# Performance work log

Hardware: AMD Instinct MI355X
Metric: run time of the kernel (lower is better)

The kernel has to match this reference:

```python
import jax, jax.numpy as jnp
import numpy as np

EMB = 1024
HEADS = 16
HEAD_DIM = EMB // HEADS  # 64


def setup_inputs() -> dict:
    key = jax.random.key(0)
    ks = jax.random.split(key, 11)
    B, S = 2, 2048
    scale = 1.0 / np.sqrt(EMB)
    inp = {
        "xv": jax.random.normal(ks[0], (B, S, EMB), jnp.float32),
        "xk": jax.random.normal(ks[1], (B, S, EMB), jnp.float32),
        "xq": jax.random.normal(ks[2], (B, S, EMB), jnp.float32),
        "Wq": jax.random.normal(ks[3], (EMB, EMB), jnp.float32) * scale,
        "bq": jax.random.normal(ks[4], (EMB,), jnp.float32) * 0.01,
        "Wk": jax.random.normal(ks[5], (EMB, EMB), jnp.float32) * scale,
        "bk": jax.random.normal(ks[6], (EMB,), jnp.float32) * 0.01,
        "Wv": jax.random.normal(ks[7], (EMB, EMB), jnp.float32) * scale,
        "bv": jax.random.normal(ks[8], (EMB,), jnp.float32) * 0.01,
        "Wo": jax.random.normal(ks[9], (EMB, EMB), jnp.float32) * scale,
        "bo": jax.random.normal(ks[10], (EMB,), jnp.float32) * 0.01,
    }
    return inp


def reference(xv, xk, xq, Wq, bq, Wk, bk, Wv, bv, Wo, bo):
    B, S, E = xq.shape
    H, D = HEADS, HEAD_DIM
    # projections (x @ W + b), split into heads: [B,S,H,D]
    Q = (xq @ Wq + bq).reshape(B, S, H, D)
    K = (xk @ Wk + bk).reshape(B, S, H, D)
    V = (xv @ Wv + bv).reshape(B, S, H, D)
    # scaled dot-product attention per head (vectorized over heads)
    scores = jnp.einsum("bqhd,bkhd->bhqk", Q, K) / jnp.sqrt(jnp.float32(D))
    attn = jax.nn.softmax(scores, axis=-1)
    ctx = jnp.einsum("bhqk,bkhd->bqhd", attn, V).reshape(B, S, E)
    return ctx @ Wo + bo
```

## Files before the change

### kernel.cpp

```cpp
#include <hip/hip_runtime.h>
#include <hip/hip_bf16.h>

typedef __hip_bfloat16 bf16;
typedef __attribute__((ext_vector_type(8))) short short8;
typedef __attribute__((ext_vector_type(4))) short short4v;
typedef __attribute__((ext_vector_type(4))) float floatx4;

#define MFMA16 __builtin_amdgcn_mfma_f32_16x16x32_bf16
#define BARRIER __builtin_amdgcn_s_barrier
#define SCHEDB0() __builtin_amdgcn_sched_barrier(0)
#define SETPRIO __builtin_amdgcn_s_setprio


__device__ __forceinline__ void gl16(const void* g, void* l) {
    __builtin_amdgcn_global_load_lds(
        (const __attribute__((address_space(1))) void*)g,
        (__attribute__((address_space(3))) void*)l, 16, 0, 0);
}

__global__ __launch_bounds__(256) void prep_k(const float* __restrict__ w0,
                                              const float* __restrict__ w1,
                                              const float* __restrict__ w2,
                                              const float* __restrict__ w3,
                                              bf16* __restrict__ wdst,
                                              const float* __restrict__ x0,
                                              const float* __restrict__ x1,
                                              const float* __restrict__ x2,
                                              bf16* __restrict__ xdst) {
    int bid = blockIdx.x, tid = threadIdx.x;
    if (bid < 4096) {
        const float* srcs[4] = {w0, w1, w2, w3};
        int z = bid >> 10, by = (bid >> 5) & 31, bx = bid & 31;
        const float* src = srcs[z];
        bf16* d = wdst + (size_t)z * 1024 * 1024;
        __shared__ float t[32][33];
        int tx = tid & 31, ty = tid >> 5;
        int x0c = bx * 32, y0 = by * 32;
#pragma unroll
        for (int i = 0; i < 4; i++)
            t[ty + i * 8][tx] = src[(size_t)(y0 + ty + i * 8) * 1024 + x0c + tx];
        __syncthreads();
#pragma unroll
        for (int i = 0; i < 4; i++)
            d[(size_t)(x0c + ty + i * 8) * 1024 + y0 + tx] =
                __float2bfloat16(t[tx][ty + i * 8]);
    } else {
        int ib = bid - 4096;
        int zc = ib >> 11, blk = ib & 2047;
        const float* srcs[3] = {x0, x1, x2};
        const float* src = srcs[zc];
        bf16* d = xdst + (size_t)zc * (4096 * 1024);
        size_t i = (size_t)blk * 256 + tid;
        const float4* s4 = (const float4*)src + i * 2;
        float4 a = s4[0], b = s4[1];
        union { __hip_bfloat162 h2[4]; short8 s; } pk;
        pk.h2[0] = __float22bfloat162_rn(make_float2(a.x, a.y));
        pk.h2[1] = __float22bfloat162_rn(make_float2(a.z, a.w));
        pk.h2[2] = __float22bfloat162_rn(make_float2(b.x, b.y));
        pk.h2[3] = __float22bfloat162_rn(make_float2(b.z, b.w));
        *(short8*)&d[i * 8] = pk.s;
    }
}

__global__ __launch_bounds__(256) void qkv_k(const bf16* __restrict__ xb,
                                             const bf16* __restrict__ wt,
                                             const float* __restrict__ bq,
                                             const float* __restrict__ bk,
                                             const float* __restrict__ bv,
                                             bf16* __restrict__ Qw,
                                             bf16* __restrict__ Kw,
                                             bf16* __restrict__ Vt) {
    __shared__ __align__(16) bf16 lA[3][128 * 32];
    __shared__ __align__(16) bf16 lB[3][128 * 32];
    int z = blockIdx.z;
    const bf16* A = xb + (size_t)z * (4096 * 1024);
    const bf16* Bt = wt + (size_t)z * (1024 * 1024);
    const float* bias = (z == 0) ? bq : (z == 1) ? bk : bv;
    int m0 = blockIdx.x * 128, n0 = blockIdx.y * 128;
    int tid = threadIdx.x, wave = tid >> 6, lane = tid & 63;
    int lm = lane & 15, quad = lane >> 4;
    int wm = wave >> 1, wn = wave & 1;
    int swb = quad ^ ((lm >> 1) & 3);

    floatx4 acc[4][4];
#pragma unroll
    for (int i = 0; i < 4; i++)
#pragma unroll
        for (int j = 0; j < 4; j++) acc[i][j] = (floatx4){0.f, 0.f, 0.f, 0.f};

    auto stage = [&](int bufi, int kt) {
#pragma unroll
        for (int q2 = 0; q2 < 2; q2++) {
            int slot0 = wave * 128 + q2 * 64;
            int r = (slot0 + lane) >> 2;
            int c = (lane & 3) ^ ((r >> 1) & 3);
            gl16(&A[(size_t)(m0 + r) * 1024 + kt * 32 + c * 8],
                 &lA[bufi][slot0 * 8]);
            gl16(&Bt[(size_t)(n0 + r) * 1024 + kt * 32 + c * 8],
                 &lB[bufi][slot0 * 8]);
        }
    };

    auto compute = [&](int cur) {
        short8 af[4], bfr[4];
#pragma unroll
        for (int ms = 0; ms < 4; ms++) {
            int r = wm * 64 + ms * 16 + lm;
            af[ms] = *(const short8*)&lA[cur][(r * 4 + swb) * 8];
        }
#pragma unroll
        for (int ns = 0; ns < 4; ns++) {
            int r = wn * 64 + ns * 16 + lm;
            bfr[ns] = *(const short8*)&lB[cur][(r * 4 + swb) * 8];
        }
        SETPRIO(1);
#pragma unroll
        for (int ms = 0; ms < 4; ms++)
#pragma unroll
            for (int ns = 0; ns < 4; ns++)
                acc[ms][ns] = MFMA16(af[ms], bfr[ns], acc[ms][ns], 0, 0, 0);
        SETPRIO(0);
    };

    stage(0, 0);
    stage(1, 1);
    for (int kt = 0; kt < 32; kt++) {
        int cur = kt % 3;
        BARRIER();
        if (kt < 30) {
            stage((kt + 2) % 3, kt + 2);
            asm volatile("s_waitcnt vmcnt(8)" ::: "memory");
        } else if (kt == 30) {
            asm volatile("s_waitcnt vmcnt(4)" ::: "memory");
        } else {
            asm volatile("s_waitcnt vmcnt(0)" ::: "memory");
        }
        BARRIER();
        SCHEDB0();
        compute(cur);
    }

    bf16* dstQK = (z == 0) ? Qw : Kw;
    float scale = (z == 0) ? 0.125f * 1.44269504f : 1.0f;
#pragma unroll
    for (int ms = 0; ms < 4; ms++) {
        int rowb = m0 + wm * 64 + ms * 16 + quad * 4;
        int bb = rowb >> 11, s0 = rowb & 2047;
#pragma unroll
        for (int ns = 0; ns < 4; ns++) {
            int col = n0 + wn * 64 + ns * 16 + lm;
            float bvv = bias[col];
            int hh = col >> 6, d = col & 63;
            if (z < 2) {
#pragma unroll
                for (int rr = 0; rr < 4; rr++) {
                    float v = (acc[ms][ns][rr] + bvv) * scale;
                    dstQK[((((size_t)bb * 16 + hh) * 2048 + s0 + rr) << 6) + d] =
                        __float2bfloat16(v);
                }
            } else {
                short4v pk;
#pragma unroll
                for (int rr = 0; rr < 4; rr++) {
                    bf16 h = __float2bfloat16(acc[ms][ns][rr] + bvv);
                    pk[rr] = *(short*)&h;
                }
                *(short4v*)&Vt[((((size_t)bb * 16 + hh) * 64 + d) << 11) + s0] = pk;
            }
        }
    }
}

__global__ __launch_bounds__(256) void outproj_k(const bf16* __restrict__ ctx,
                                                 const bf16* __restrict__ wot,
                                                 const float* __restrict__ bo,
                                                 float* __restrict__ out) {
    __shared__ __align__(16) bf16 lA[2][128 * 32];
    __shared__ __align__(16) bf16 lB[2][64 * 32];
    int m0 = blockIdx.x * 128, n0 = blockIdx.y * 64;
    int tid = threadIdx.x, wave = tid >> 6, lane = tid & 63;
    int lm = lane & 15, quad = lane >> 4;
    int wm = wave >> 1, wn = wave & 1;
    int swb = quad ^ ((lm >> 1) & 3);

    floatx4 acc[4][2];
#pragma unroll
    for (int i = 0; i < 4; i++)
#pragma unroll
        for (int j = 0; j < 2; j++) acc[i][j] = (floatx4){0.f, 0.f, 0.f, 0.f};

    auto stage = [&](int bufi, int kt) {
#pragma unroll
        for (int q2 = 0; q2 < 2; q2++) {
            int slot0 = wave * 128 + q2 * 64;
            int r = (slot0 + lane) >> 2;
            int c = (lane & 3) ^ ((r >> 1) & 3);
            gl16(&ctx[(size_t)(m0 + r) * 1024 + kt * 32 + c * 8],
                 &lA[bufi][slot0 * 8]);
        }
        {
            int slot0 = wave * 64;
            int r = (slot0 + lane) >> 2;
            int c = (lane & 3) ^ ((r >> 1) & 3);
            gl16(&wot[(size_t)(n0 + r) * 1024 + kt * 32 + c * 8],
                 &lB[bufi][slot0 * 8]);
        }
    };

    auto compute = [&](int cur) {
        short8 af[4], bfr[2];
#pragma unroll
        for (int ms = 0; ms < 4; ms++) {
            int r = wm * 64 + ms * 16 + lm;
            af[ms] = *(const short8*)&lA[cur][(r * 4 + swb) * 8];
        }
#pragma unroll
        for (int ns = 0; ns < 2; ns++) {
            int r = wn * 32 + ns * 16 + lm;
            bfr[ns] = *(const short8*)&lB[cur][(r * 4 + swb) * 8];
        }
        SETPRIO(1);
#pragma unroll
        for (int ms = 0; ms < 4; ms++)
#pragma unroll
            for (int ns = 0; ns < 2; ns++)
                acc[ms][ns] = MFMA16(af[ms], bfr[ns], acc[ms][ns], 0, 0, 0);
        SETPRIO(0);
    };

    stage(0, 0);
    for (int kt = 0; kt < 31; kt++) {
        int cur = kt & 1;
        BARRIER();
        stage(cur ^ 1, kt + 1);
        asm volatile("s_waitcnt vmcnt(3)" ::: "memory");
        BARRIER();
        SCHEDB0();
        compute(cur);
    }
    BARRIER();
    asm volatile("s_waitcnt vmcnt(0)" ::: "memory");
    BARRIER();
    SCHEDB0();
    compute(1);

#pragma unroll
    for (int ms = 0; ms < 4; ms++) {
        int rowb = m0 + wm * 64 + ms * 16 + quad * 4;
#pragma unroll
        for (int ns = 0; ns < 2; ns++) {
            int col = n0 + wn * 32 + ns * 16 + lm;
            float bvv = bo[col];
#pragma unroll
            for (int rr = 0; rr < 4; rr++)
                out[(size_t)(rowb + rr) * 1024 + col] = acc[ms][ns][rr] + bvv;
        }
    }
}

__global__ __launch_bounds__(512, 4) void attn_k(const bf16* __restrict__ Q,
                                                 const bf16* __restrict__ K,
                                                 const bf16* __restrict__ Vt,
                                                 bf16* __restrict__ ctx) {
    __shared__ __align__(16) bf16 lK[2][128 * 64];
    __shared__ __align__(16) bf16 lV[2][64 * 128];
    __shared__ float scrL[4][32];
    int bh = blockIdx.x, qt = blockIdx.y;
    int b = bh >> 4, h = bh & 15;
    const bf16* Qh = Q + (size_t)bh * (2048 * 64);
    const bf16* Kh = K + (size_t)bh * (2048 * 64);
    const bf16* Vh = Vt + (size_t)bh * (64 * 2048);
    int tid = threadIdx.x, wave = tid >> 6, lane = tid & 63;
    int lm = lane & 15, quad = lane >> 4;
    int s7 = lm & 7;
    int wq = wave >> 1, wk = wave & 1;

    short8 qf[2][2];
#pragma unroll
    for (int qblk = 0; qblk < 2; qblk++) {
        int qrow = qt * 128 + wq * 32 + qblk * 16 + lm;
        qf[qblk][0] = *(const short8*)&Qh[(size_t)qrow * 64 + quad * 8];
        qf[qblk][1] = *(const short8*)&Qh[(size_t)qrow * 64 + 32 + quad * 8];
    }

    short8 onesf;
#pragma unroll
    for (int i = 0; i < 8; i++) onesf[i] = (short)0x3F80;

    floatx4 o[2][4];
#pragma unroll
    for (int i = 0; i < 2; i++)
#pragma unroll
        for (int j = 0; j < 4; j++) o[i][j] = (floatx4){0.f, 0.f, 0.f, 0.f};
    floatx4 accL[2];
#pragma unroll
    for (int i = 0; i < 2; i++) accL[i] = (floatx4){0.f, 0.f, 0.f, 0.f};

    auto stage = [&](int bufi, int kt) {
#pragma unroll
        for (int q2 = 0; q2 < 2; q2++) {
            int slot0 = wave * 128 + q2 * 64;
            int r = (slot0 + lane) >> 3;
            int c = (lane & 7) ^ (r & 7);
            gl16(&Kh[(size_t)(kt * 128 + r) * 64 + c * 8], &lK[bufi][slot0 * 8]);
        }
#pragma unroll
        for (int q2 = 0; q2 < 2; q2++) {
            int slot0 = wave * 128 + q2 * 64;
            int s = slot0 + lane;
            int r = s >> 4, cl = s & 15;
            int c = cl ^ (r & 7);
            gl16(&Vh[(size_t)r * 2048 + kt * 128 + c * 8], &lV[bufi][slot0 * 8]);
        }
    };

    auto compute = [&](int cur) {
#pragma unroll
        for (int half = 0; half < 2; half++) {
            short8 kf[2][2];
#pragma unroll
            for (int ksub = 0; ksub < 2; ksub++) {
                int r = wk * 64 + half * 32 + ksub * 16 + lm;
#pragma unroll
                for (int ds = 0; ds < 2; ds++)
                    kf[ksub][ds] = *(const short8*)
                        &lK[cur][(r * 8 + ((ds * 4 + quad) ^ s7)) * 8];
            }
            floatx4 s[2][2];
#pragma unroll
            for (int i = 0; i < 2; i++)
#pragma unroll
                for (int j = 0; j < 2; j++) s[i][j] = (floatx4){0.f, 0.f, 0.f, 0.f};
            SETPRIO(1);
#pragma unroll
            for (int qblk = 0; qblk < 2; qblk++)
#pragma unroll
                for (int ksub = 0; ksub < 2; ksub++) {
                    s[qblk][ksub] = MFMA16(kf[ksub][0], qf[qblk][0], s[qblk][ksub], 0, 0, 0);
                    s[qblk][ksub] = MFMA16(kf[ksub][1], qf[qblk][1], s[qblk][ksub], 0, 0, 0);
                }
            SETPRIO(0);

            short8 pz[2];
#pragma unroll
            for (int qblk = 0; qblk < 2; qblk++) {
                union { short4v h[2]; short8 s8; } up;
#pragma unroll
                for (int ksub = 0; ksub < 2; ksub++) {
                    float p0 = __builtin_amdgcn_exp2f(s[qblk][ksub][0]);
                    float p1 = __builtin_amdgcn_exp2f(s[qblk][ksub][1]);
                    float p2 = __builtin_amdgcn_exp2f(s[qblk][ksub][2]);
                    float p3 = __builtin_amdgcn_exp2f(s[qblk][ksub][3]);
                    union { __hip_bfloat162 b2[2]; short4v s4; } c;
                    c.b2[0] = __float22bfloat162_rn(make_float2(p0, p1));
                    c.b2[1] = __float22bfloat162_rn(make_float2(p2, p3));
                    up.h[ksub] = c.s4;
                }
                pz[qblk] = up.s8;
            }

            short8 vfz[4];
#pragma unroll
            for (int dblk = 0; dblk < 4; dblk++) {
                int d = dblk * 16 + lm;
                union { short4v h[2]; short8 s8; } uv;
#pragma unroll
                for (int ksub = 0; ksub < 2; ksub++) {
                    int c = wk * 8 + half * 4 + ksub * 2 + (quad >> 1);
                    uv.h[ksub] = *(const short4v*)
                        &lV[cur][(d * 16 + (c ^ s7)) * 8 + (quad & 1) * 4];
                }
                vfz[dblk] = uv.s8;
            }

            SETPRIO(1);
#pragma unroll
            for (int qblk = 0; qblk < 2; qblk++) {
                accL[qblk] = MFMA16(pz[qblk], onesf, accL[qblk], 0, 0, 0);
#pragma unroll
                for (int dblk = 0; dblk < 4; dblk++)
                    o[qblk][dblk] = MFMA16(pz[qblk], vfz[dblk], o[qblk][dblk], 0, 0, 0);
            }
            SETPRIO(0);
        }
    };

    stage(0, 0);
    for (int kt = 0; kt < 15; kt++) {
        int cur = kt & 1;
        BARRIER();
        stage(cur ^ 1, kt + 1);
        asm volatile("s_waitcnt vmcnt(4)" ::: "memory");
        BARRIER();
        SCHEDB0();
        compute(cur);
    }
    BARRIER();
    asm volatile("s_waitcnt vmcnt(0)" ::: "memory");
    BARRIER();
    SCHEDB0();
    compute(1);

    __syncthreads();
    float* scrO = (float*)&lK[0][0];
    if (wk == 1) {
#pragma unroll
        for (int qblk = 0; qblk < 2; qblk++) {
#pragma unroll
            for (int dblk = 0; dblk < 4; dblk++)
#pragma unroll
                for (int rr = 0; rr < 4; rr++)
                    scrO[wq * 2048 + (qblk * 16 + quad * 4 + rr) * 64 +
                         dblk * 16 + lm] = o[qblk][dblk][rr];
#pragma unroll
            for (int rr = 0; rr < 4; rr++)
                scrL[wq][qblk * 16 + quad * 4 + rr] = accL[qblk][rr];
        }
    }
    __syncthreads();
    if (wk == 0) {
#pragma unroll
        for (int qblk = 0; qblk < 2; qblk++) {
            float inv[4];
#pragma unroll
            for (int rr = 0; rr < 4; rr++)
                inv[rr] = 1.f / (accL[qblk][rr] +
                                 scrL[wq][qblk * 16 + quad * 4 + rr]);
#pragma unroll
            for (int dblk = 0; dblk < 4; dblk++) {
                int e = h * 64 + dblk * 16 + lm;
#pragma unroll
                for (int rr = 0; rr < 4; rr++) {
                    int srow = qt * 128 + wq * 32 + qblk * 16 + quad * 4 + rr;
                    float of = o[qblk][dblk][rr] +
                               scrO[wq * 2048 + (qblk * 16 + quad * 4 + rr) * 64 +
                                    dblk * 16 + lm];
                    ctx[(size_t)(b * 2048 + srow) * 1024 + e] =
                        __float2bfloat16(of * inv[rr]);
                }
            }
        }
    }
}

extern "C" void kernel_launch(void* const* d_in, const int* in_sizes, int n_in,
                              void* d_out, int out_size, void* d_ws, size_t ws_size,
                              hipStream_t stream) {
    const float* xv = (const float*)d_in[0];
    const float* xk = (const float*)d_in[1];
    const float* xq = (const float*)d_in[2];
    const float* Wq = (const float*)d_in[3];
    const float* bq = (const float*)d_in[4];
    const float* Wk = (const float*)d_in[5];
    const float* bk = (const float*)d_in[6];
    const float* Wv = (const float*)d_in[7];
    const float* bv = (const float*)d_in[8];
    const float* Wo = (const float*)d_in[9];
    const float* bo = (const float*)d_in[10];
    float* out = (float*)d_out;
    bf16* ws = (bf16*)d_ws;

    const size_t MB1 = 1024 * 1024;
    bf16* wt  = ws;
    bf16* Qw  = ws + 4 * MB1;
    bf16* Kw  = ws + 8 * MB1;
    bf16* Vt  = ws + 12 * MB1;
    bf16* ctx = ws + 16 * MB1;
    bf16* xb  = ws + 20 * MB1;

    hipLaunchKernelGGL(prep_k, dim3(10240), dim3(256), 0, stream,
                       Wq, Wk, Wv, Wo, wt, xq, xk, xv, xb);

    hipLaunchKernelGGL(qkv_k, dim3(32, 8, 3), dim3(256), 0, stream,
                       xb, wt, bq, bk, bv, Qw, Kw, Vt);

    hipLaunchKernelGGL(attn_k, dim3(32, 16), dim3(512), 0, stream, Qw, Kw, Vt, ctx);

    hipLaunchKernelGGL(outproj_k, dim3(32, 16), dim3(256), 0, stream,
                       ctx, wt + 3 * MB1, bo, out);
}
```

Measured before the change: 210.0 us.

## Interleave QK and PV halves in attention; shrink out-proj tile to 64x64

The attention compute is restructured so the second half's QK MFMAs and K fragment reads are issued while the first half's exponentials and PV MFMAs are still in progress. This software pipelining is meant to hide exp and LDS latency behind matrix work, at the cost of more live registers under the 4-block launch bound. Separately, the output projection tile shrinks from 128x64 to 64x64 and the grid doubles, giving more blocks to fill the CUs. The trade-off there is lower data reuse per block.

```diff
diff --git a/kernel.cpp b/kernel.cpp
--- a/kernel.cpp
+++ b/kernel.cpp
@@ -175,43 +175,35 @@
                                                  const bf16* __restrict__ wot,
                                                  const float* __restrict__ bo,
                                                  float* __restrict__ out) {
-    __shared__ __align__(16) bf16 lA[2][128 * 32];
+    __shared__ __align__(16) bf16 lA[2][64 * 32];
     __shared__ __align__(16) bf16 lB[2][64 * 32];
-    int m0 = blockIdx.x * 128, n0 = blockIdx.y * 64;
+    int m0 = blockIdx.x * 64, n0 = blockIdx.y * 64;
     int tid = threadIdx.x, wave = tid >> 6, lane = tid & 63;
     int lm = lane & 15, quad = lane >> 4;
     int wm = wave >> 1, wn = wave & 1;
     int swb = quad ^ ((lm >> 1) & 3);
 
-    floatx4 acc[4][2];
-#pragma unroll
-    for (int i = 0; i < 4; i++)
+    floatx4 acc[2][2];
+#pragma unroll
+    for (int i = 0; i < 2; i++)
 #pragma unroll
         for (int j = 0; j < 2; j++) acc[i][j] = (floatx4){0.f, 0.f, 0.f, 0.f};
 
     auto stage = [&](int bufi, int kt) {
-#pragma unroll
-        for (int q2 = 0; q2 < 2; q2++) {
-            int slot0 = wave * 128 + q2 * 64;
-            int r = (slot0 + lane) >> 2;
-            int c = (lane & 3) ^ ((r >> 1) & 3);
-            gl16(&ctx[(size_t)(m0 + r) * 1024 + kt * 32 + c * 8],
-                 &lA[bufi][slot0 * 8]);
-        }
-        {
-            int slot0 = wave * 64;
-            int r = (slot0 + lane) >> 2;
-            int c = (lane & 3) ^ ((r >> 1) & 3);
-            gl16(&wot[(size_t)(n0 + r) * 1024 + kt * 32 + c * 8],
-                 &lB[bufi][slot0 * 8]);
-        }
+        int slot0 = wave * 64;
+        int r = (slot0 + lane) >> 2;
+        int c = (lane & 3) ^ ((r >> 1) & 3);
+        gl16(&ctx[(size_t)(m0 + r) * 1024 + kt * 32 + c * 8],
+             &lA[bufi][slot0 * 8]);
+        gl16(&wot[(size_t)(n0 + r) * 1024 + kt * 32 + c * 8],
+             &lB[bufi][slot0 * 8]);
     };
 
     auto compute = [&](int cur) {
-        short8 af[4], bfr[2];
-#pragma unroll
-        for (int ms = 0; ms < 4; ms++) {
-            int r = wm * 64 + ms * 16 + lm;
+        short8 af[2], bfr[2];
+#pragma unroll
+        for (int ms = 0; ms < 2; ms++) {
+            int r = wm * 32 + ms * 16 + lm;
             af[ms] = *(const short8*)&lA[cur][(r * 4 + swb) * 8];
         }
 #pragma unroll
@@ -221,7 +213,7 @@
         }
         SETPRIO(1);
 #pragma unroll
-        for (int ms = 0; ms < 4; ms++)
+        for (int ms = 0; ms < 2; ms++)
 #pragma unroll
             for (int ns = 0; ns < 2; ns++)
                 acc[ms][ns] = MFMA16(af[ms], bfr[ns], acc[ms][ns], 0, 0, 0);
@@ -233,7 +225,7 @@
         int cur = kt & 1;
         BARRIER();
         stage(cur ^ 1, kt + 1);
-        asm volatile("s_waitcnt vmcnt(3)" ::: "memory");
+        asm volatile("s_waitcnt vmcnt(2)" ::: "memory");
         BARRIER();
         SCHEDB0();
         compute(cur);
@@ -245,8 +237,8 @@
     compute(1);
 
 #pragma unroll
-    for (int ms = 0; ms < 4; ms++) {
-        int rowb = m0 + wm * 64 + ms * 16 + quad * 4;
+    for (int ms = 0; ms < 2; ms++) {
+        int rowb = m0 + wm * 32 + ms * 16 + quad * 4;
 #pragma unroll
         for (int ns = 0; ns < 2; ns++) {
             int col = n0 + wn * 32 + ns * 16 + lm;
@@ -314,75 +306,91 @@
         }
     };
 
+    auto read_kf = [&](int cur, int half, short8 kf[2][2]) {
+#pragma unroll
+        for (int ksub = 0; ksub < 2; ksub++) {
+            int r = wk * 64 + half * 32 + ksub * 16 + lm;
+#pragma unroll
+            for (int ds = 0; ds < 2; ds++)
+                kf[ksub][ds] = *(const short8*)
+                    &lK[cur][(r * 8 + ((ds * 4 + quad) ^ s7)) * 8];
+        }
+    };
+    auto qk = [&](short8 kf[2][2], floatx4 s[2][2]) {
+#pragma unroll
+        for (int i = 0; i < 2; i++)
+#pragma unroll
+            for (int j = 0; j < 2; j++) s[i][j] = (floatx4){0.f, 0.f, 0.f, 0.f};
+        SETPRIO(1);
+#pragma unroll
+        for (int qblk = 0; qblk < 2; qblk++)
+#pragma unroll
+            for (int ksub = 0; ksub < 2; ksub++) {
+                s[qblk][ksub] = MFMA16(kf[ksub][0], qf[qblk][0], s[qblk][ksub], 0, 0, 0);
+                s[qblk][ksub] = MFMA16(kf[ksub][1], qf[qblk][1], s[qblk][ksub], 0, 0, 0);
+            }
+        SETPRIO(0);
+    };
+    auto mkpz = [&](floatx4 s[2][2], short8 pz[2]) {
+#pragma unroll
+        for (int qblk = 0; qblk < 2; qblk++) {
+            union { short4v h[2]; short8 s8; } up;
+#pragma unroll
+            for (int ksub = 0; ksub < 2; ksub++) {
+                float p0 = __builtin_amdgcn_exp2f(s[qblk][ksub][0]);
+                float p1 = __builtin_amdgcn_exp2f(s[qblk][ksub][1]);
+                float p2 = __builtin_amdgcn_exp2f(s[qblk][ksub][2]);
+                float p3 = __builtin_amdgcn_exp2f(s[qblk][ksub][3]);
+                union { __hip_bfloat162 b2[2]; short4v s4; } c;
+                c.b2[0] = __float22bfloat162_rn(make_float2(p0, p1));
+                c.b2[1] = __float22bfloat162_rn(make_float2(p2, p3));
+                up.h[ksub] = c.s4;
+            }
+            pz[qblk] = up.s8;
+        }
+    };
+    auto read_vfz = [&](int cur, int half, short8 vfz[4]) {
+#pragma unroll
+        for (int dblk = 0; dblk < 4; dblk++) {
+            int d = dblk * 16 + lm;
+            union { short4v h[2]; short8 s8; } uv;
+#pragma unroll
+            for (int ksub = 0; ksub < 2; ksub++) {
+                int c = wk * 8 + half * 4 + ksub * 2 + (quad >> 1);
+                uv.h[ksub] = *(const short4v*)
+                    &lV[cur][(d * 16 + (c ^ s7)) * 8 + (quad & 1) * 4];
+            }
+            vfz[dblk] = uv.s8;
+        }
+    };
+    auto pv = [&](short8 pz[2], short8 vfz[4]) {
+        SETPRIO(1);
+#pragma unroll
+        for (int qblk = 0; qblk < 2; qblk++) {
+            accL[qblk] = MFMA16(pz[qblk], onesf, accL[qblk], 0, 0, 0);
+#pragma unroll
+            for (int dblk = 0; dblk < 4; dblk++)
+                o[qblk][dblk] = MFMA16(pz[qblk], vfz[dblk], o[qblk][dblk], 0, 0, 0);
+        }
+        SETPRIO(0);
+    };
+
     auto compute = [&](int cur) {
-#pragma unroll
-        for (int half = 0; half < 2; half++) {
-            short8 kf[2][2];
-#pragma unroll
-            for (int ksub = 0; ksub < 2; ksub++) {
-                int r = wk * 64 + half * 32 + ksub * 16 + lm;
-#pragma unroll
-                for (int ds = 0; ds < 2; ds++)
-                    kf[ksub][ds] = *(const short8*)
-                        &lK[cur][(r * 8 + ((ds * 4 + quad) ^ s7)) * 8];
-            }
-            floatx4 s[2][2];
-#pragma unroll
-            for (int i = 0; i < 2; i++)
-#pragma unroll
-                for (int j = 0; j < 2; j++) s[i][j] = (floatx4){0.f, 0.f, 0.f, 0.f};
-            SETPRIO(1);
-#pragma unroll
-            for (int qblk = 0; qblk < 2; qblk++)
-#pragma unroll
-                for (int ksub = 0; ksub < 2; ksub++) {
-                    s[qblk][ksub] = MFMA16(kf[ksub][0], qf[qblk][0], s[qblk][ksub], 0, 0, 0);
-                    s[qblk][ksub] = MFMA16(kf[ksub][1], qf[qblk][1], s[qblk][ksub], 0, 0, 0);
-                }
-            SETPRIO(0);
-
-            short8 pz[2];
-#pragma unroll
-            for (int qblk = 0; qblk < 2; qblk++) {
-                union { short4v h[2]; short8 s8; } up;
-#pragma unroll
-                for (int ksub = 0; ksub < 2; ksub++) {
-                    float p0 = __builtin_amdgcn_exp2f(s[qblk][ksub][0]);
-                    float p1 = __builtin_amdgcn_exp2f(s[qblk][ksub][1]);
-                    float p2 = __builtin_amdgcn_exp2f(s[qblk][ksub][2]);
-                    float p3 = __builtin_amdgcn_exp2f(s[qblk][ksub][3]);
-                    union { __hip_bfloat162 b2[2]; short4v s4; } c;
-                    c.b2[0] = __float22bfloat162_rn(make_float2(p0, p1));
-                    c.b2[1] = __float22bfloat162_rn(make_float2(p2, p3));
-                    up.h[ksub] = c.s4;
-                }
-                pz[qblk] = up.s8;
-            }
-
-            short8 vfz[4];
-#pragma unroll
-            for (int dblk = 0; dblk < 4; dblk++) {
-                int d = dblk * 16 + lm;
-                union { short4v h[2]; short8 s8; } uv;
-#pragma unroll
-                for (int ksub = 0; ksub < 2; ksub++) {
-                    int c = wk * 8 + half * 4 + ksub * 2 + (quad >> 1);
-                    uv.h[ksub] = *(const short4v*)
-                        &lV[cur][(d * 16 + (c ^ s7)) * 8 + (quad & 1) * 4];
-                }
-                vfz[dblk] = uv.s8;
-            }
-
-            SETPRIO(1);
-#pragma unroll
-            for (int qblk = 0; qblk < 2; qblk++) {
-                accL[qblk] = MFMA16(pz[qblk], onesf, accL[qblk], 0, 0, 0);
-#pragma unroll
-                for (int dblk = 0; dblk < 4; dblk++)
-                    o[qblk][dblk] = MFMA16(pz[qblk], vfz[dblk], o[qblk][dblk], 0, 0, 0);
-            }
-            SETPRIO(0);
-        }
+        short8 kf0[2][2], kf1[2][2];
+        floatx4 s0[2][2], s1[2][2];
+        short8 pz0[2], pz1[2];
+        short8 vfz0[4], vfz1[4];
+
+        read_kf(cur, 0, kf0);
+        qk(kf0, s0);
+        read_kf(cur, 1, kf1);
+        mkpz(s0, pz0);
+        qk(kf1, s1);
+        read_vfz(cur, 0, vfz0);
+        pv(pz0, vfz0);
+        mkpz(s1, pz1);
+        read_vfz(cur, 1, vfz1);
+        pv(pz1, vfz1);
     };
 
     stage(0, 0);
@@ -476,6 +484,6 @@
 
     hipLaunchKernelGGL(attn_k, dim3(32, 16), dim3(512), 0, stream, Qw, Kw, Vt, ctx);
 
-    hipLaunchKernelGGL(outproj_k, dim3(32, 16), dim3(256), 0, stream,
+    hipLaunchKernelGGL(outproj_k, dim3(64, 16), dim3(256), 0, stream,
                        ctx, wt + 3 * MB1, bo, out);
 }
```

Result: slower. 216.2 us (+2.9%).
